# Kernel tuning notes

Hardware: AMD Instinct MI355X
Metric: run time of the kernel (lower is better)

## Reference

```python
import jax, jax.numpy as jnp
import numpy as np

# Module config (from init_kwargs)
B, S = 2, 2048            # batch, prompt length
NH, D = 16, 64            # num query heads, head_size
NKV = 4                   # num kv heads
QPK = NH // NKV           # queries per kv head (GQA)
BLOCK = 128               # paged KV-cache block size
NBLOCKS = 64              # total cache blocks
SCALE = 0.125             # 1/sqrt(D)
NEG = -1e9                # causal mask value (finite for grad safety)


def setup_inputs() -> dict:
    key = jax.random.key(0)
    k1, k2, k3 = jax.random.split(key, 3)
    query = jax.random.normal(k1, (B, S, NH * D), jnp.float32)
    key_t = jax.random.normal(k2, (B, S, NKV * D), jnp.float32)
    value = jax.random.normal(k3, (B, S, NKV * D), jnp.float32)
    # kv_cache = [2, num_blocks, block_size, num_kv_heads, head_size]
    kv_cache = jnp.zeros((2, NBLOCKS, BLOCK, NKV, D), jnp.float32)
    # causal attn_bias [B, 1, 1, S, S] as set by the vLLM model runner
    i = jnp.arange(S)
    causal = jnp.where(i[None, :] <= i[:, None], 0.0, NEG).astype(jnp.float32)
    attn_bias = jnp.broadcast_to(causal[None, None, None], (B, 1, 1, S, S))
    # standard alibi slopes for 16 heads: 2^(-0.5*(h+1))
    alibi_slopes = 2.0 ** (-0.5 * (jnp.arange(NH, dtype=jnp.float32) + 1.0))
    # prompt writes B*S/BLOCK = 32 full blocks into the cache
    block_indices = jnp.arange(B * S // BLOCK, dtype=jnp.int32)
    return {"query": query, "key": key_t, "value": value, "kv_cache": kv_cache,
            "attn_bias": attn_bias, "alibi_slopes": alibi_slopes,
            "block_indices": block_indices}


def reference(query, key, value, kv_cache, attn_bias, alibi_slopes, block_indices):
    Bq, Sq, _ = query.shape
    q = query.reshape(Bq, Sq, NKV, QPK, D)   # [b, i, h, g, d]
    k = key.reshape(Bq, Sq, NKV, D)          # [b, j, h, d]
    v = value.reshape(Bq, Sq, NKV, D)

    # --- paged KV-cache scatter (VLLMKVCache.insert_or_update_cache, prompt path) ---
    k_blocks = key.reshape(-1, BLOCK, NKV, D)   # [n_used_blocks, block, h, d]
    v_blocks = value.reshape(-1, BLOCK, NKV, D)
    key_cache = kv_cache[0].at[block_indices].set(k_blocks)
    value_cache = kv_cache[1].at[block_indices].set(v_blocks)

    # --- _make_alibi_bias: (j - i) * slope, unflattened to [1, Hkv, qpk, S, S] ---
    ar = jnp.arange(Sq)
    diff = (ar[None, :] - ar[:, None]).astype(query.dtype)        # [S, S]
    pos_bias = alibi_slopes[:, None, None] * diff                  # [NH, S, S]
    pos_bias = pos_bias.reshape(1, NKV, QPK, Sq, Sq)
    bias = attn_bias + pos_bias                                    # [B, Hkv, qpk, S, S]

    # --- prompt_attention: matmul_qk -> softmax -> matmul_av (GQA) ---
    scores = jnp.einsum('bihgd,bjhd->bhgij', q, k) * SCALE + bias
    attn = jax.nn.softmax(scores, axis=-1)
    out = jnp.einsum('bhgij,bjhd->bihgd', attn, v).reshape(Bq, Sq, NH * D)
    return out, key_cache, value_cache
```

## Files before the change

### kernel.cpp

```cpp
#include <hip/hip_runtime.h>
#include <hip/hip_bf16.h>
#include <math.h>

#define BB    2
#define SS    2048
#define NHh   16
#define DD    64
#define NKV   4
#define BLKV  128
#define SCALE 0.125f

#define KT    64

typedef __attribute__((ext_vector_type(8))) short short8;
typedef __attribute__((ext_vector_type(4))) float f32x4;
typedef __attribute__((ext_vector_type(4))) int   i32x4;

template<int N> struct IC { static constexpr int v = N; };

__device__ inline short bf16c(float x) {
  __hip_bfloat16 h = __float2bfloat16(x);
  return *reinterpret_cast<short*>(&h);
}

__device__ inline int pk_bf16(float a, float b) {
  int d;
  asm("v_cvt_pk_bf16_f32 %0, %1, %2" : "=v"(d) : "v"(a), "v"(b));
  return d;
}

#define GLL16(g, l) __builtin_amdgcn_global_load_lds( \
    (const __attribute__((address_space(1))) void*)(g), \
    (__attribute__((address_space(3))) void*)(l), 16, 0, 0)

__global__ __launch_bounds__(256) void aux_kernel(
    const float* __restrict__ k, const float* __restrict__ v,
    const float* __restrict__ kvc, const int* __restrict__ bidx, int nidx,
    unsigned short* __restrict__ kimg, unsigned short* __restrict__ vimg,
    float* __restrict__ kc, float* __restrict__ vc)
{
  const int wg  = blockIdx.x;
  const int tid = threadIdx.x;
  if (wg < BB * NKV * (SS / KT)) {
    const int t   = wg & 31;
    const int hkv = (wg >> 5) & 3;
    const int b   = wg >> 7;
    const int j0  = t * KT;
    const float* kp = k + ((size_t)(b * SS + j0) * NKV + hkv) * DD;
    const float* vp = v + ((size_t)(b * SS + j0) * NKV + hkv) * DD;
    unsigned short* ki = kimg + (size_t)wg * 4096;
    unsigned short* vi = vimg + (size_t)wg * 4096;
    const int bi    = bidx[b * 16 + (t >> 1)];
    const int rowc0 = (t & 1) * 64;
    float* kcb = kc + (size_t)bi * (BLKV * NKV * DD);
    float* vcb = vc + (size_t)bi * (BLKV * NKV * DD);

    {
      const int jj = tid >> 2;
      const int sb = (tid & 3) * 2;
#pragma unroll
      for (int ss = 0; ss < 2; ++ss) {
        const int s  = sb + ss;
        const int d0 = (s ^ (jj & 7)) * 8;
        const float4 a = *(const float4*)(kp + jj * (NKV * DD) + d0);
        const float4 c = *(const float4*)(kp + jj * (NKV * DD) + d0 + 4);
        *(short8*)&ki[jj * 64 + s * 8] =
            (short8){bf16c(a.x), bf16c(a.y), bf16c(a.z), bf16c(a.w),
                     bf16c(c.x), bf16c(c.y), bf16c(c.z), bf16c(c.w)};
        float* kd = kcb + (rowc0 + jj) * (NKV * DD) + hkv * DD + d0;
        *(float4*)kd       = a;
        *(float4*)(kd + 4) = c;
      }
    }
    {
      const int d = tid & 63;
      const int w = tid >> 6;
#pragma unroll
      for (int ji = 0; ji < 2; ++ji) {
        const int jb = w * 2 + ji;
        float vv[8];
#pragma unroll
        for (int e = 0; e < 8; ++e)
          vv[e] = vp[(jb * 8 + e) * (NKV * DD) + d];
        const int s = jb ^ (d & 7);
        *(short8*)&vi[d * 64 + s * 8] =
            (short8){bf16c(vv[0]), bf16c(vv[1]), bf16c(vv[2]), bf16c(vv[3]),
                     bf16c(vv[4]), bf16c(vv[5]), bf16c(vv[6]), bf16c(vv[7])};
#pragma unroll
        for (int e = 0; e < 8; ++e)
          vcb[(rowc0 + jb * 8 + e) * (NKV * DD) + hkv * DD + d] = vv[e];
      }
    }
  } else {
    const int w2    = wg - BB * NKV * (SS / KT);
    const int blk   = w2 & 63;
    const int plane = w2 >> 6;
    int covered = 0;
    for (int m = 0; m < nidx; ++m) covered |= (bidx[m] == blk);
    if (covered) return;
    const float4* s4 = (const float4*)(kvc + (size_t)plane * (64 * BLKV * NKV * DD)
                                           + (size_t)blk * (BLKV * NKV * DD));
    float4* d4 = (float4*)((plane ? vc : kc) + (size_t)blk * (BLKV * NKV * DD));
#pragma unroll 4
    for (int i = tid; i < (BLKV * NKV * DD) / 4; i += 256) d4[i] = s4[i];
  }
}

__global__ __launch_bounds__(256) void attn_kernel(
    const float* __restrict__ q, const unsigned short* __restrict__ kimg,
    const unsigned short* __restrict__ vimg, const float* __restrict__ slopes,
    float* __restrict__ out)
{
  __shared__ __align__(16) unsigned short Kbuf[2][4096];
  __shared__ __align__(16) unsigned short Vbuf[2][4096];

  const int tid  = threadIdx.x;
  const int wave = tid >> 6;
  const int lane = tid & 63;
  const int cl   = lane & 15;
  const int g    = lane >> 4;

  const int grp   = blockIdx.x & 7;
  const int b     = grp >> 2;
  const int hkv   = grp & 3;
  const int local = blockIdx.x >> 3;
  const int h     = hkv * 4 + (local & 3);
  const int qt    = 31 - (local >> 2);

  const float L2E    = 1.44269504088896340736f;
  const float slope2 = slopes[h] * L2E;
  const float SC2    = SCALE * L2E;
  const int q_blk = qt * 64;
  const int q0    = q_blk + wave * 16;
  const int iq    = q0 + cl;

  short8 qf[2];
  {
    const float* qp = q + ((size_t)(b * SS + iq) * NHh + h) * DD;
#pragma unroll
    for (int kq = 0; kq < 2; ++kq) {
      const int d0 = kq * 32 + g * 8;
      const float4 a = *(const float4*)(qp + d0);
      const float4 c = *(const float4*)(qp + d0 + 4);
      qf[kq] = (short8){bf16c(a.x), bf16c(a.y), bf16c(a.z), bf16c(a.w),
                        bf16c(c.x), bf16c(c.y), bf16c(c.z), bf16c(c.w)};
    }
  }

  const float slope16 = slope2 * 16.f;
  const float slope64 = slope2 * 64.f;
  float ab = -slope2 * (float)iq;
  float cst[4];
#pragma unroll
  for (int r = 0; r < 4; ++r) cst[r] = slope2 * (float)(4 * g + r);

  const int src0 = cl + ((g & 1) << 5);
  const int src1 = src0 + 16;
  const bool gEven = (g < 2);

  float m_ = -INFINITY, l_ = 0.f;
  f32x4 acc[4];
#pragma unroll
  for (int dt = 0; dt < 4; ++dt) acc[dt] = (f32x4){0.f, 0.f, 0.f, 0.f};

  const char* kt0 = (const char*)kimg + (size_t)((b * NKV + hkv) * 32) * 8192;
  const char* vt0 = (const char*)vimg + (size_t)((b * NKV + hkv) * 32) * 8192;
  const int goff0 = wave * 2048 + lane * 16;
  const int ldst0 = wave * 2048;

  auto stage = [&](auto BUFC, int t) {
    constexpr int B = decltype(BUFC)::v;
    const char* kt = kt0 + (size_t)t * 8192 + goff0;
    const char* vt = vt0 + (size_t)t * 8192 + goff0;
    GLL16(kt,        (char*)&Kbuf[B][0] + ldst0);
    GLL16(kt + 1024, (char*)&Kbuf[B][0] + ldst0 + 1024);
    GLL16(vt,        (char*)&Vbuf[B][0] + ldst0);
    GLL16(vt + 1024, (char*)&Vbuf[B][0] + ldst0 + 1024);
  };

  auto tile = [&](auto BUFC, auto MSKC, int t) {
    constexpr int B    = decltype(BUFC)::v;
    constexpr bool MSK = decltype(MSKC)::v;
    const unsigned short* Kb = Kbuf[B];
    const unsigned short* Vb = Vbuf[B];

    f32x4 sc[4];
    __builtin_amdgcn_s_setprio(1);
#pragma unroll
    for (int jt = 0; jt < 4; ++jt) {
      const int rb = (jt * 16 + cl) * 64;
      const short8 kfA = *(const short8*)&Kb[rb + ((g       ^ (cl & 7)) << 3)];
      const short8 kfB = *(const short8*)&Kb[rb + (((4 | g) ^ (cl & 7)) << 3)];
      f32x4 s = (f32x4){0.f, 0.f, 0.f, 0.f};
      s = __builtin_amdgcn_mfma_f32_16x16x32_bf16(kfA, qf[0], s, 0, 0, 0);
      s = __builtin_amdgcn_mfma_f32_16x16x32_bf16(kfB, qf[1], s, 0, 0, 0);
      sc[jt] = s;
    }
    __builtin_amdgcn_s_setprio(0);

    float pm = -INFINITY;
#pragma unroll
    for (int jt = 0; jt < 4; ++jt) {
      const float ajt = ab + slope16 * (float)jt;
#pragma unroll
      for (int r = 0; r < 4; ++r) {
        float val = fmaf(sc[jt][r], SC2, ajt + cst[r]);
        if (MSK) {
          const int j = t * 64 + jt * 16 + 4 * g + r;
          val = (j <= iq) ? val : -INFINITY;
        }
        sc[jt][r] = val;
        pm = fmaxf(pm, val);
      }
    }
    pm = fmaxf(pm, __shfl_xor(pm, 16));
    pm = fmaxf(pm, __shfl_xor(pm, 32));

    if (!__all(pm - m_ <= 11.5f)) {
      const float mn = fmaxf(m_, pm);
      const float sf = exp2f(m_ - mn);
      m_ = mn;
      l_ *= sf;
#pragma unroll
      for (int dt = 0; dt < 4; ++dt)
#pragma unroll
        for (int r = 0; r < 4; ++r) acc[dt][r] *= sf;
    }

    float rs = 0.f;
#pragma unroll
    for (int jt = 0; jt < 4; ++jt) {
#pragma unroll
      for (int r = 0; r < 4; ++r) {
        const float p = exp2f(sc[jt][r] - m_);
        sc[jt][r] = p;
        rs += p;
      }
    }
    rs += __shfl_xor(rs, 16);
    rs += __shfl_xor(rs, 32);
    l_ += rs;

    __builtin_amdgcn_s_setprio(1);
#pragma unroll
    for (int ks = 0; ks < 2; ++ks) {
      const int E0 = pk_bf16(sc[2 * ks][0],     sc[2 * ks][1]);
      const int E1 = pk_bf16(sc[2 * ks][2],     sc[2 * ks][3]);
      const int O0 = pk_bf16(sc[2 * ks + 1][0], sc[2 * ks + 1][1]);
      const int O1 = pk_bf16(sc[2 * ks + 1][2], sc[2 * ks + 1][3]);
      const int d0e = __shfl(E0, src0), d0o = __shfl(O0, src0);
      const int d1e = __shfl(E1, src0), d1o = __shfl(O1, src0);
      const int d2e = __shfl(E0, src1), d2o = __shfl(O0, src1);
      const int d3e = __shfl(E1, src1), d3o = __shfl(O1, src1);
      i32x4 pd;
      pd[0] = gEven ? d0e : d0o;
      pd[1] = gEven ? d1e : d1o;
      pd[2] = gEven ? d2e : d2o;
      pd[3] = gEven ? d3e : d3o;
      const short8 pb = *(const short8*)&pd;
#pragma unroll
      for (int dt = 0; dt < 4; ++dt) {
        const short8 va = *(const short8*)
            &Vb[(dt * 16 + cl) * 64 + ((((ks << 2) | g) ^ (cl & 7)) << 3)];
        acc[dt] = __builtin_amdgcn_mfma_f32_16x16x32_bf16(va, pb, acc[dt], 0, 0, 0);
      }
    }
    __builtin_amdgcn_s_setprio(0);

    ab += slope64;
  };

  stage(IC<0>{}, 0);
  __syncthreads();

  const int nt = qt + 1;
  const int NU = nt - 1;
  int t = 0;
  while (t + 2 <= NU) {
    stage(IC<1>{}, t + 1);
    tile(IC<0>{}, IC<0>{}, t);
    __syncthreads();
    stage(IC<0>{}, t + 2);
    tile(IC<1>{}, IC<0>{}, t + 1);
    __syncthreads();
    t += 2;
  }
  if (t < NU) {
    stage(IC<1>{}, t + 1);
    tile(IC<0>{}, IC<0>{}, t);
    __syncthreads();
    tile(IC<1>{}, IC<1>{}, t + 1);
  } else {
    tile(IC<0>{}, IC<1>{}, t);
  }

  const float inv = 1.f / l_;
  float* op = out + ((size_t)(b * SS + iq) * NHh + h) * DD + 4 * g;
#pragma unroll
  for (int dt = 0; dt < 4; ++dt) {
    float4 o4;
    o4.x = acc[dt][0] * inv;
    o4.y = acc[dt][1] * inv;
    o4.z = acc[dt][2] * inv;
    o4.w = acc[dt][3] * inv;
    *(float4*)(op + dt * 16) = o4;
  }
}

extern "C" void kernel_launch(void* const* d_in, const int* in_sizes, int n_in,
                              void* d_out, int out_size, void* d_ws, size_t ws_size,
                              hipStream_t stream) {
  const float* q      = (const float*)d_in[0];
  const float* k      = (const float*)d_in[1];
  const float* v      = (const float*)d_in[2];
  const float* kvc    = (const float*)d_in[3];
  const float* slopes = (const float*)d_in[5];
  const int*   bidx   = (const int*)d_in[6];

  float* out = (float*)d_out;
  float* kc  = out + BB * SS * NHh * DD;
  float* vc  = kc + 64 * BLKV * NKV * DD;

  unsigned short* kimg = (unsigned short*)d_ws;
  unsigned short* vimg = kimg + (size_t)BB * NKV * 32 * 4096;

  const int nidx = in_sizes[6];

  aux_kernel<<<dim3(256 + 128), dim3(256), 0, stream>>>(
      k, v, kvc, bidx, nidx, kimg, vimg, kc, vc);

  attn_kernel<<<dim3(1024), dim3(256), 0, stream>>>(q, kimg, vimg, slopes, out);
}
```

Baseline: 65.62 us.

## Triple-buffer KV tiles with single barrier and route P through LDS

```diff
diff --git a/kernel.cpp b/kernel.cpp
--- a/kernel.cpp
+++ b/kernel.cpp
@@ -11,22 +11,15 @@
 #define SCALE 0.125f
 
 #define KT    64
+#define LDP   72
 
 typedef __attribute__((ext_vector_type(8))) short short8;
+typedef __attribute__((ext_vector_type(4))) short short4v;
 typedef __attribute__((ext_vector_type(4))) float f32x4;
-typedef __attribute__((ext_vector_type(4))) int   i32x4;
-
-template<int N> struct IC { static constexpr int v = N; };
 
 __device__ inline short bf16c(float x) {
   __hip_bfloat16 h = __float2bfloat16(x);
   return *reinterpret_cast<short*>(&h);
-}
-
-__device__ inline int pk_bf16(float a, float b) {
-  int d;
-  asm("v_cvt_pk_bf16_f32 %0, %1, %2" : "=v"(d) : "v"(a), "v"(b));
-  return d;
 }
 
 #define GLL16(g, l) __builtin_amdgcn_global_load_lds( \
@@ -111,8 +104,10 @@
     const unsigned short* __restrict__ vimg, const float* __restrict__ slopes,
     float* __restrict__ out)
 {
-  __shared__ __align__(16) unsigned short Kbuf[2][4096];
-  __shared__ __align__(16) unsigned short Vbuf[2][4096];
+  __shared__ __align__(16) unsigned short Kbuf[3][4096];
+  __shared__ __align__(16) unsigned short Vbuf[3][4096];
+  __shared__ __align__(16) unsigned short P_lds[4][16 * LDP];
+  __shared__ float sf_lds[4][16];
 
   const int tid  = threadIdx.x;
   const int wave = tid >> 6;
@@ -154,10 +149,6 @@
 #pragma unroll
   for (int r = 0; r < 4; ++r) cst[r] = slope2 * (float)(4 * g + r);
 
-  const int src0 = cl + ((g & 1) << 5);
-  const int src1 = src0 + 16;
-  const bool gEven = (g < 2);
-
   float m_ = -INFINITY, l_ = 0.f;
   f32x4 acc[4];
 #pragma unroll
@@ -168,22 +159,17 @@
   const int goff0 = wave * 2048 + lane * 16;
   const int ldst0 = wave * 2048;
 
-  auto stage = [&](auto BUFC, int t) {
-    constexpr int B = decltype(BUFC)::v;
+  auto stage = [&](unsigned short* kb, unsigned short* vb, int t) {
     const char* kt = kt0 + (size_t)t * 8192 + goff0;
     const char* vt = vt0 + (size_t)t * 8192 + goff0;
-    GLL16(kt,        (char*)&Kbuf[B][0] + ldst0);
-    GLL16(kt + 1024, (char*)&Kbuf[B][0] + ldst0 + 1024);
-    GLL16(vt,        (char*)&Vbuf[B][0] + ldst0);
-    GLL16(vt + 1024, (char*)&Vbuf[B][0] + ldst0 + 1024);
+    GLL16(kt,        (char*)kb + ldst0);
+    GLL16(kt + 1024, (char*)kb + ldst0 + 1024);
+    GLL16(vt,        (char*)vb + ldst0);
+    GLL16(vt + 1024, (char*)vb + ldst0 + 1024);
   };
 
-  auto tile = [&](auto BUFC, auto MSKC, int t) {
-    constexpr int B    = decltype(BUFC)::v;
-    constexpr bool MSK = decltype(MSKC)::v;
-    const unsigned short* Kb = Kbuf[B];
-    const unsigned short* Vb = Vbuf[B];
-
+  auto tile = [&](const unsigned short* Kb, const unsigned short* Vb,
+                  int t, bool masked) {
     f32x4 sc[4];
     __builtin_amdgcn_s_setprio(1);
 #pragma unroll
@@ -205,7 +191,7 @@
 #pragma unroll
       for (int r = 0; r < 4; ++r) {
         float val = fmaf(sc[jt][r], SC2, ajt + cst[r]);
-        if (MSK) {
+        if (masked) {
           const int j = t * 64 + jt * 16 + 4 * g + r;
           val = (j <= iq) ? val : -INFINITY;
         }
@@ -221,48 +207,41 @@
       const float sf = exp2f(m_ - mn);
       m_ = mn;
       l_ *= sf;
+      if (g == 0) sf_lds[wave][cl] = sf;
+      asm volatile("s_waitcnt lgkmcnt(0)" ::: "memory");
+      const f32x4 sfq = *(const f32x4*)&sf_lds[wave][4 * g];
 #pragma unroll
       for (int dt = 0; dt < 4; ++dt)
 #pragma unroll
-        for (int r = 0; r < 4; ++r) acc[dt][r] *= sf;
+        for (int r = 0; r < 4; ++r) acc[dt][r] *= sfq[r];
     }
 
     float rs = 0.f;
 #pragma unroll
     for (int jt = 0; jt < 4; ++jt) {
-#pragma unroll
-      for (int r = 0; r < 4; ++r) {
-        const float p = exp2f(sc[jt][r] - m_);
-        sc[jt][r] = p;
-        rs += p;
-      }
+      const float p0 = exp2f(sc[jt][0] - m_);
+      const float p1 = exp2f(sc[jt][1] - m_);
+      const float p2 = exp2f(sc[jt][2] - m_);
+      const float p3 = exp2f(sc[jt][3] - m_);
+      rs += p0 + p1 + p2 + p3;
+      *(short4v*)&P_lds[wave][cl * LDP + jt * 16 + 4 * g] =
+          (short4v){bf16c(p0), bf16c(p1), bf16c(p2), bf16c(p3)};
     }
     rs += __shfl_xor(rs, 16);
     rs += __shfl_xor(rs, 32);
     l_ += rs;
 
+    asm volatile("s_waitcnt lgkmcnt(0)" ::: "memory");
+
     __builtin_amdgcn_s_setprio(1);
 #pragma unroll
     for (int ks = 0; ks < 2; ++ks) {
-      const int E0 = pk_bf16(sc[2 * ks][0],     sc[2 * ks][1]);
-      const int E1 = pk_bf16(sc[2 * ks][2],     sc[2 * ks][3]);
-      const int O0 = pk_bf16(sc[2 * ks + 1][0], sc[2 * ks + 1][1]);
-      const int O1 = pk_bf16(sc[2 * ks + 1][2], sc[2 * ks + 1][3]);
-      const int d0e = __shfl(E0, src0), d0o = __shfl(O0, src0);
-      const int d1e = __shfl(E1, src0), d1o = __shfl(O1, src0);
-      const int d2e = __shfl(E0, src1), d2o = __shfl(O0, src1);
-      const int d3e = __shfl(E1, src1), d3o = __shfl(O1, src1);
-      i32x4 pd;
-      pd[0] = gEven ? d0e : d0o;
-      pd[1] = gEven ? d1e : d1o;
-      pd[2] = gEven ? d2e : d2o;
-      pd[3] = gEven ? d3e : d3o;
-      const short8 pb = *(const short8*)&pd;
+      const short8 pa = *(const short8*)&P_lds[wave][cl * LDP + ks * 32 + g * 8];
 #pragma unroll
       for (int dt = 0; dt < 4; ++dt) {
-        const short8 va = *(const short8*)
+        const short8 vb = *(const short8*)
             &Vb[(dt * 16 + cl) * 64 + ((((ks << 2) | g) ^ (cl & 7)) << 3)];
-        acc[dt] = __builtin_amdgcn_mfma_f32_16x16x32_bf16(va, pb, acc[dt], 0, 0, 0);
+        acc[dt] = __builtin_amdgcn_mfma_f32_16x16x32_bf16(pa, vb, acc[dt], 0, 0, 0);
       }
     }
     __builtin_amdgcn_s_setprio(0);
@@ -270,40 +249,36 @@
     ab += slope64;
   };
 
-  stage(IC<0>{}, 0);
-  __syncthreads();
-
   const int nt = qt + 1;
-  const int NU = nt - 1;
-  int t = 0;
-  while (t + 2 <= NU) {
-    stage(IC<1>{}, t + 1);
-    tile(IC<0>{}, IC<0>{}, t);
-    __syncthreads();
-    stage(IC<0>{}, t + 2);
-    tile(IC<1>{}, IC<0>{}, t + 1);
-    __syncthreads();
-    t += 2;
+  stage(Kbuf[0], Vbuf[0], 0);
+  if (nt > 1) stage(Kbuf[1], Vbuf[1], 1);
+
+  unsigned short *ka = Kbuf[0], *kb2 = Kbuf[1], *kc2 = Kbuf[2];
+  unsigned short *va = Vbuf[0], *vb2 = Vbuf[1], *vc2 = Vbuf[2];
+
+  for (int t = 0; t < nt; ++t) {
+    if (t + 1 < nt) {
+      asm volatile("s_waitcnt vmcnt(4)" ::: "memory");
+    } else {
+      asm volatile("s_waitcnt vmcnt(0)" ::: "memory");
+    }
+    __builtin_amdgcn_sched_barrier(0);
+    __builtin_amdgcn_s_barrier();
+    if (t + 2 < nt) stage(kc2, vc2, t + 2);
+    tile(ka, va, t, t == nt - 1);
+    unsigned short* tk = ka; ka = kb2; kb2 = kc2; kc2 = tk;
+    unsigned short* tv = va; va = vb2; vb2 = vc2; vc2 = tv;
   }
-  if (t < NU) {
-    stage(IC<1>{}, t + 1);
-    tile(IC<0>{}, IC<0>{}, t);
-    __syncthreads();
-    tile(IC<1>{}, IC<1>{}, t + 1);
-  } else {
-    tile(IC<0>{}, IC<1>{}, t);
-  }
-
-  const float inv = 1.f / l_;
-  float* op = out + ((size_t)(b * SS + iq) * NHh + h) * DD + 4 * g;
-#pragma unroll
-  for (int dt = 0; dt < 4; ++dt) {
-    float4 o4;
-    o4.x = acc[dt][0] * inv;
-    o4.y = acc[dt][1] * inv;
-    o4.z = acc[dt][2] * inv;
-    o4.w = acc[dt][3] * inv;
-    *(float4*)(op + dt * 16) = o4;
+
+  if (g == 0) sf_lds[wave][cl] = l_;
+  asm volatile("s_waitcnt lgkmcnt(0)" ::: "memory");
+  const f32x4 lq = *(const f32x4*)&sf_lds[wave][4 * g];
+#pragma unroll
+  for (int r = 0; r < 4; ++r) {
+    const float inv = 1.f / lq[r];
+    float* op = out + ((size_t)(b * SS + q0 + 4 * g + r) * NHh + h) * DD;
+#pragma unroll
+    for (int dt = 0; dt < 4; ++dt) op[dt * 16 + cl] = acc[r == 0 ? dt : dt][r] * inv;
   }
 }
 
```

Result: slower. 74.34 us (+13.3%).
